# Kernel optimization log

Measured on AMD Instinct MI355X. Metric: run time of the kernel, lower is better.

The kernel has to match this reference:

```python
import jax, jax.numpy as jnp
import numpy as np

# NF4 codebook (bitsandbytes)
NF4 = jnp.array([-1.0, -0.6961928009986877, -0.5250730514526367, -0.39491748809814453,
                 -0.28444138169288635, -0.18477343022823334, -0.09105003625154495, 0.0,
                 0.07958029955625534, 0.16093020141124725, 0.24611230194568634,
                 0.33791524171829224, 0.44070982933044434, 0.5626170039176941,
                 0.7229568362236023, 1.0], dtype=jnp.float32)
BLOCK = 64  # quantization blocksize along the input dim


def _dequant(codes, scales):
    # codes: [O, I] int in [0,16); scales: [O, I//BLOCK] per-block absmax
    w = NF4[codes]                                   # [O, I]
    O, I = w.shape
    w = w.reshape(O, I // BLOCK, BLOCK) * scales[:, :, None]
    return w.reshape(O, I)


def _lin_lora(x, W, A, B):
    # base int4 linear + low-rank adapter: x @ W.T + (x @ A.T) @ B.T
    base = jnp.einsum('bsh,oh->bso', x, W)
    lora = jnp.einsum('bsr,or->bso', jnp.einsum('bsh,rh->bsr', x, A), B)
    return base + lora


def setup_inputs() -> dict:
    H, I, R, BT, S = 4096, 14336, 16, 2, 2048
    key = jax.random.key(0)
    ks = jax.random.split(key, 12)
    x = jax.random.normal(ks[0], (BT, S, H), jnp.float32)
    codes_attn = jax.random.randint(ks[1], (4, H, H), 0, 16, jnp.int32)
    scales_attn = jax.random.uniform(ks[2], (4, H, H // BLOCK), jnp.float32) * 0.02
    codes_gu = jax.random.randint(ks[3], (2, I, H), 0, 16, jnp.int32)
    scales_gu = jax.random.uniform(ks[4], (2, I, H // BLOCK), jnp.float32) * 0.02
    codes_down = jax.random.randint(ks[5], (H, I), 0, 16, jnp.int32)
    scales_down = jax.random.uniform(ks[6], (H, I // BLOCK), jnp.float32) * 0.02
    lora_A_h = jax.random.normal(ks[7], (6, R, H), jnp.float32) * 0.02
    lora_A_down = jax.random.normal(ks[8], (R, I), jnp.float32) * 0.02
    lora_B_attn = jax.random.normal(ks[9], (4, H, R), jnp.float32) * 0.02
    lora_B_gu = jax.random.normal(ks[10], (2, I, R), jnp.float32) * 0.02
    lora_B_down = jax.random.normal(ks[11], (H, R), jnp.float32) * 0.02
    return dict(x=x, codes_attn=codes_attn, scales_attn=scales_attn,
                codes_gu=codes_gu, scales_gu=scales_gu,
                codes_down=codes_down, scales_down=scales_down,
                lora_A_h=lora_A_h, lora_A_down=lora_A_down,
                lora_B_attn=lora_B_attn, lora_B_gu=lora_B_gu,
                lora_B_down=lora_B_down)


def reference(x, codes_attn, scales_attn, codes_gu, scales_gu, codes_down,
              scales_down, lora_A_h, lora_A_down, lora_B_attn, lora_B_gu,
              lora_B_down):
    # attention projections (q, k, v)
    q = _lin_lora(x, _dequant(codes_attn[0], scales_attn[0]), lora_A_h[0], lora_B_attn[0])
    k = _lin_lora(x, _dequant(codes_attn[1], scales_attn[1]), lora_A_h[1], lora_B_attn[1])
    v = _lin_lora(x, _dequant(codes_attn[2], scales_attn[2]), lora_A_h[2], lora_B_attn[2])
    attn = (q + k + v) / 3.0
    o = _lin_lora(attn, _dequant(codes_attn[3], scales_attn[3]), lora_A_h[3], lora_B_attn[3])
    x1 = x + o
    # MLP: silu(gate) * up -> down
    g = _lin_lora(x1, _dequant(codes_gu[0], scales_gu[0]), lora_A_h[4], lora_B_gu[0])
    u = _lin_lora(x1, _dequant(codes_gu[1], scales_gu[1]), lora_A_h[5], lora_B_gu[1])
    h = jax.nn.silu(g) * u
    d = _lin_lora(h, _dequant(codes_down, scales_down), lora_A_down, lora_B_down)
    return x1 + d
```

## Files before the change

kernel.cpp:

```cpp
#include <hip/hip_runtime.h>
#include <cstdint>


typedef __attribute__((ext_vector_type(4))) float f32x4;
typedef __attribute__((ext_vector_type(8))) short s16x8;
typedef __attribute__((ext_vector_type(4))) int   i32x4;

__constant__ float NF4_TBL[16] = {
  -1.0f, -0.6961928009986877f, -0.5250730514526367f, -0.39491748809814453f,
  -0.28444138169288635f, -0.18477343022823334f, -0.09105003625154495f, 0.0f,
   0.07958029955625534f, 0.16093020141124725f, 0.24611230194568634f,
   0.33791524171829224f, 0.44070982933044434f, 0.5626170039176941f,
   0.7229568362236023f, 1.0f };

__device__ __forceinline__ unsigned short f2bf(float f){
  unsigned u = __builtin_bit_cast(unsigned, f);
  u += 0x7fffu + ((u >> 16) & 1u);
  return (unsigned short)(u >> 16);
}
__device__ __forceinline__ float bf2f(unsigned short h){
  return __builtin_bit_cast(float, ((unsigned)h) << 16);
}

__device__ __forceinline__ void gll16(const unsigned short* g, unsigned short* l){
  __builtin_amdgcn_global_load_lds((__attribute__((address_space(1))) unsigned int*)g,
                                   (__attribute__((address_space(3))) unsigned int*)l,
                                   16, 0, 0);
}

__global__ void cast_f32_bf16(unsigned short* __restrict__ dst,
                              const float* __restrict__ src, long long n8){
  const long long i = (long long)blockIdx.x * blockDim.x + threadIdx.x;
  if (i >= n8) return;
  const f32x4 a = *(const f32x4*)(src + i*8);
  const f32x4 b = *(const f32x4*)(src + i*8 + 4);
  s16x8 o;
  o[0]=(short)f2bf(a.x); o[1]=(short)f2bf(a.y); o[2]=(short)f2bf(a.z); o[3]=(short)f2bf(a.w);
  o[4]=(short)f2bf(b.x); o[5]=(short)f2bf(b.y); o[6]=(short)f2bf(b.z); o[7]=(short)f2bf(b.w);
  *(s16x8*)(dst + i*8) = o;
}

__global__ void pack_bl_kernel(unsigned short* __restrict__ dst,
                               const float* __restrict__ src,
                               int N, int coloff, float mul){
  const int i = blockIdx.x * blockDim.x + threadIdx.x;
  if (i >= N * 16) return;
  const int n = i >> 4, r = i & 15;
  dst[(size_t)n * 64 + coloff + r] = f2bf(src[i] * mul);
}

__global__ void dequant1_kernel(unsigned short* __restrict__ dst,
                                const int* __restrict__ codes,
                                const float* __restrict__ scales, int K, float mul){
  const int k = (blockIdx.x * blockDim.x + threadIdx.x) * 8;
  if (k >= K) return;
  const size_t n = blockIdx.y;
  const size_t base = n * (size_t)K + k;
  const float s = scales[n * (size_t)(K >> 6) + (k >> 6)] * mul;
  const i32x4 c0 = *(const i32x4*)(codes + base);
  const i32x4 c1 = *(const i32x4*)(codes + base + 4);
  s16x8 o;
  o[0]=(short)f2bf(NF4_TBL[c0.x]*s); o[1]=(short)f2bf(NF4_TBL[c0.y]*s);
  o[2]=(short)f2bf(NF4_TBL[c0.z]*s); o[3]=(short)f2bf(NF4_TBL[c0.w]*s);
  o[4]=(short)f2bf(NF4_TBL[c1.x]*s); o[5]=(short)f2bf(NF4_TBL[c1.y]*s);
  o[6]=(short)f2bf(NF4_TBL[c1.z]*s); o[7]=(short)f2bf(NF4_TBL[c1.w]*s);
  *(s16x8*)(dst + base) = o;
}

__global__ void dequant3_kernel(unsigned short* __restrict__ dst,
                                const int* __restrict__ codes,
                                const float* __restrict__ scales, int K, float mul){
  const int k = (blockIdx.x * blockDim.x + threadIdx.x) * 8;
  if (k >= K) return;
  const size_t n = blockIdx.y;
  const size_t base = n * (size_t)K + k;
  const size_t CS = (size_t)4096 * 4096;
  const size_t SS = (size_t)4096 * 64;
  float acc[8] = {0.f,0.f,0.f,0.f,0.f,0.f,0.f,0.f};
  #pragma unroll
  for (int t = 0; t < 3; ++t){
    const float s = scales[t * SS + n * (size_t)(K >> 6) + (k >> 6)];
    const i32x4 c0 = *(const i32x4*)(codes + t * CS + base);
    const i32x4 c1 = *(const i32x4*)(codes + t * CS + base + 4);
    acc[0]+=NF4_TBL[c0.x]*s; acc[1]+=NF4_TBL[c0.y]*s; acc[2]+=NF4_TBL[c0.z]*s; acc[3]+=NF4_TBL[c0.w]*s;
    acc[4]+=NF4_TBL[c1.x]*s; acc[5]+=NF4_TBL[c1.y]*s; acc[6]+=NF4_TBL[c1.z]*s; acc[7]+=NF4_TBL[c1.w]*s;
  }
  s16x8 o;
  #pragma unroll
  for (int e = 0; e < 8; ++e) o[e] = (short)f2bf(acc[e] * mul);
  *(s16x8*)(dst + base) = o;
}

template<int NP>
__global__ __launch_bounds__(256)
void lora_t_kernel(const unsigned short* __restrict__ act,
                   const unsigned short* __restrict__ Ab,
                   unsigned short* __restrict__ tout, int K, int coloff){
  __shared__ float red[4][NP][4][64];
  const int tid = threadIdx.x, lane = tid & 63, wave = tid >> 6;
  const int m0 = blockIdx.x * 16;
  const int q = lane >> 4, r = lane & 15;
  const int KW = K >> 2;
  const int kbase = wave * KW;
  const unsigned short* ap = act + (size_t)(m0 + r) * K + kbase + q * 8;
  const unsigned short* bp[NP];
  #pragma unroll
  for (int p = 0; p < NP; ++p)
    bp[p] = Ab + (size_t)(p * 16 + r) * K + kbase + q * 8;
  f32x4 acc[NP];
  #pragma unroll
  for (int p = 0; p < NP; ++p) acc[p] = (f32x4){0.f,0.f,0.f,0.f};
  for (int k = 0; k < KW; k += 32){
    const s16x8 a = *(const s16x8*)ap; ap += 32;
    #pragma unroll
    for (int p = 0; p < NP; ++p){
      const s16x8 b = *(const s16x8*)bp[p]; bp[p] += 32;
      acc[p] = __builtin_amdgcn_mfma_f32_16x16x32_bf16(a, b, acc[p], 0, 0, 0);
    }
  }
  #pragma unroll
  for (int p = 0; p < NP; ++p)
    #pragma unroll
    for (int rr = 0; rr < 4; ++rr) red[wave][p][rr][lane] = acc[p][rr];
  __syncthreads();
  const int rr = tid >> 6, li = tid & 63;
  #pragma unroll
  for (int p = 0; p < NP; ++p){
    const float v = red[0][p][rr][li] + red[1][p][rr][li]
                  + red[2][p][rr][li] + red[3][p][rr][li];
    const int row = m0 + (li >> 4) * 4 + rr;
    const int col = coloff + p * 16 + (li & 15);
    tout[(size_t)row * 64 + col] = f2bf(v);
  }
}

__global__ void silu_mul_kernel(unsigned short* __restrict__ h,
                                const unsigned short* __restrict__ gu){
  const int k8 = blockIdx.x * blockDim.x + threadIdx.x;
  const size_t row = blockIdx.y;
  const s16x8 g8 = *(const s16x8*)(gu + row * 28672 + (size_t)k8 * 8);
  const s16x8 u8 = *(const s16x8*)(gu + row * 28672 + 14336 + (size_t)k8 * 8);
  s16x8 o;
  #pragma unroll
  for (int e = 0; e < 8; ++e){
    const float g = bf2f((unsigned short)g8[e]);
    const float u = bf2f((unsigned short)u8[e]);
    const float s = g / (1.f + __expf(-g));
    o[e] = (short)f2bf(s * u);
  }
  *(s16x8*)(h + row * 14336 + (size_t)k8 * 8) = o;
}

template<int EPI>
__global__ __launch_bounds__(256)
void gemm_kernel(const unsigned short* __restrict__ Aact,
                 const unsigned short* __restrict__ Bw,
                 const unsigned short* __restrict__ tL,
                 const unsigned short* __restrict__ bL,
                 int K, int ldC,
                 const float* __restrict__ resIn,
                 float* __restrict__ outF,
                 unsigned short* __restrict__ outB){
  __shared__ unsigned short As[128 * 64];
  __shared__ unsigned short Bs[128 * 64];
  const int tid  = threadIdx.x;
  const int lane = tid & 63;
  const int wave = tid >> 6;
  const int m0 = blockIdx.x << 7;
  const int n0 = blockIdx.y << 7;

  const int srow  = tid >> 3;
  const int scol  = tid & 7;
  const int swcol = scol ^ (srow & 7);
  const unsigned short* gA = Aact + (size_t)(m0 + srow) * K + swcol * 8;
  const unsigned short* gB = Bw   + (size_t)(n0 + srow) * K + swcol * 8;
  const int ldsbase = wave * 512;

  const int wm = wave >> 1, wn = wave & 1;
  const int q = lane >> 4, r15 = lane & 15;
  int aoff[4][2], boff[4][2];
  #pragma unroll
  for (int i = 0; i < 4; ++i){
    const int ml = wm*64 + i*16 + r15;
    const int nl = wn*64 + i*16 + r15;
    #pragma unroll
    for (int kk = 0; kk < 2; ++kk){
      aoff[i][kk] = ml*64 + ((((kk<<2)|q) ^ (ml & 7)) * 8);
      boff[i][kk] = nl*64 + ((((kk<<2)|q) ^ (nl & 7)) * 8);
    }
  }

  f32x4 acc[4][4];
  #pragma unroll
  for (int i = 0; i < 4; ++i)
    #pragma unroll
    for (int j = 0; j < 4; ++j) acc[i][j] = (f32x4){0.f,0.f,0.f,0.f};

  const int nK = K >> 6;
  size_t koff = 0;
  for (int kt = 0; kt <= nK; ++kt){
    const unsigned short* pa; const unsigned short* pb; size_t rs;
    if (kt < nK){ pa = gA + koff; pb = gB + koff; rs = (size_t)K * 32; }
    else {
      pa = tL + (size_t)(m0 + srow) * 64 + swcol * 8;
      pb = bL + (size_t)(n0 + srow) * 64 + swcol * 8;
      rs = 64 * 32;
    }
    #pragma unroll
    for (int p = 0; p < 4; ++p){
      gll16(pa + rs * p, As + ldsbase + p * 2048);
      gll16(pb + rs * p, Bs + ldsbase + p * 2048);
    }
    __syncthreads();
    #pragma unroll
    for (int kk = 0; kk < 2; ++kk){
      s16x8 af[4], bfr[4];
      #pragma unroll
      for (int i = 0; i < 4; ++i) af[i]  = *(const s16x8*)(As + aoff[i][kk]);
      #pragma unroll
      for (int j = 0; j < 4; ++j) bfr[j] = *(const s16x8*)(Bs + boff[j][kk]);
      #pragma unroll
      for (int i = 0; i < 4; ++i)
        #pragma unroll
        for (int j = 0; j < 4; ++j)
          acc[i][j] = __builtin_amdgcn_mfma_f32_16x16x32_bf16(af[i], bfr[j], acc[i][j], 0, 0, 0);
    }
    __syncthreads();
    koff += 64;
  }

  #pragma unroll
  for (int i = 0; i < 4; ++i){
    const int gm = m0 + wm*64 + i*16 + q*4;
    #pragma unroll
    for (int j = 0; j < 4; ++j){
      const int gn = n0 + wn*64 + j*16 + r15;
      #pragma unroll
      for (int rr = 0; rr < 4; ++rr){
        const size_t idx = (size_t)(gm + rr) * ldC + gn;
        const float v = acc[i][j][rr];
        if constexpr (EPI == 0){
          outB[idx] = f2bf(v);
        } else if constexpr (EPI == 1){
          const float x1 = resIn[idx] + v;
          outF[idx] = x1;
          outB[idx] = f2bf(x1);
        } else {
          outF[idx] = resIn[idx] + v;
        }
      }
    }
  }
}

extern "C" void kernel_launch(void* const* d_in, const int* in_sizes, int n_in,
                              void* d_out, int out_size, void* d_ws, size_t ws_size,
                              hipStream_t stream){
  (void)in_sizes; (void)n_in; (void)out_size; (void)ws_size;
  constexpr int M = 4096, H = 4096, I = 14336, I2 = 28672;

  const float* x            = (const float*)d_in[0];
  const int*   codes_attn   = (const int*)  d_in[1];
  const float* scales_attn  = (const float*)d_in[2];
  const int*   codes_gu     = (const int*)  d_in[3];
  const float* scales_gu    = (const float*)d_in[4];
  const int*   codes_down   = (const int*)  d_in[5];
  const float* scales_down  = (const float*)d_in[6];
  const float* lora_A_h     = (const float*)d_in[7];
  const float* lora_A_down  = (const float*)d_in[8];
  const float* lora_B_attn  = (const float*)d_in[9];
  const float* lora_B_gu    = (const float*)d_in[10];
  const float* lora_B_down  = (const float*)d_in[11];
  float* out = (float*)d_out;

  char* ws = (char*)d_ws;
  size_t off = 0;
  auto take = [&](size_t b){ void* p = ws + off; off += b; return p; };
  unsigned short* xb    = (unsigned short*)take((size_t)M*H*2);
  unsigned short* W1    = (unsigned short*)take((size_t)H*H*2);
  unsigned short* attn  = (unsigned short*)take((size_t)M*H*2);
  float*          x1f   = (float*)         take((size_t)M*H*4);
  unsigned short* x1b   = (unsigned short*)take((size_t)M*H*2);
  unsigned short* Wgu   = (unsigned short*)take((size_t)I2*H*2);
  unsigned short* gu    = (unsigned short*)take((size_t)M*I2*2);
  unsigned short* hbuf  = (unsigned short*)take((size_t)M*I*2);
  unsigned short* t1    = (unsigned short*)take((size_t)M*64*2);
  unsigned short* t2    = (unsigned short*)take((size_t)M*64*2);
  unsigned short* t3    = (unsigned short*)take((size_t)M*64*2);
  unsigned short* t4    = (unsigned short*)take((size_t)M*64*2);
  unsigned short* bl_at = (unsigned short*)take((size_t)H*64*2);
  unsigned short* bl_o  = (unsigned short*)take((size_t)H*64*2);
  unsigned short* bl_gu = (unsigned short*)take((size_t)I2*64*2);
  unsigned short* bl_dn = (unsigned short*)take((size_t)H*64*2);
  const size_t zbytes = (size_t)((char*)ws + off - (char*)t1);
  unsigned short* al_h  = (unsigned short*)take((size_t)6*16*H*2);
  unsigned short* al_dn = (unsigned short*)take((size_t)16*I*2);

  hipMemsetAsync(t1, 0, zbytes, stream);

  cast_f32_bf16<<<dim3((M*(size_t)H/8)/256), 256, 0, stream>>>(xb, x, (long long)M*H/8);
  cast_f32_bf16<<<dim3(192), 256, 0, stream>>>(al_h,  lora_A_h,    (long long)6*16*H/8);
  cast_f32_bf16<<<dim3(112), 256, 0, stream>>>(al_dn, lora_A_down, (long long)16*I/8);

  for (int p = 0; p < 3; ++p)
    pack_bl_kernel<<<dim3(256), 256, 0, stream>>>(bl_at, lora_B_attn + (size_t)p*H*16, H, p*16, 1.f/3.f);
  pack_bl_kernel<<<dim3(256), 256, 0, stream>>>(bl_o, lora_B_attn + (size_t)3*H*16, H, 0, 1.f);
  pack_bl_kernel<<<dim3(896), 256, 0, stream>>>(bl_gu, lora_B_gu, I, 0, 1.f);
  pack_bl_kernel<<<dim3(896), 256, 0, stream>>>(bl_gu + (size_t)I*64, lora_B_gu + (size_t)I*16, I, 16, 1.f);
  pack_bl_kernel<<<dim3(256), 256, 0, stream>>>(bl_dn, lora_B_down, H, 0, 1.f);

  lora_t_kernel<3><<<dim3(M/16), 256, 0, stream>>>(xb, al_h, t1, H, 0);

  dequant3_kernel<<<dim3(H/2048, H), 256, 0, stream>>>(W1, codes_attn, scales_attn, H, 1.f/3.f);
  gemm_kernel<0><<<dim3(32, 32), 256, 0, stream>>>(xb, W1, t1, bl_at, H, H, nullptr, nullptr, attn);

  dequant1_kernel<<<dim3(H/2048, H), 256, 0, stream>>>(W1, codes_attn + (size_t)3*H*H,
                                                       scales_attn + (size_t)3*H*64, H, 1.f);
  lora_t_kernel<1><<<dim3(M/16), 256, 0, stream>>>(attn, al_h + (size_t)3*16*H, t2, H, 0);
  gemm_kernel<1><<<dim3(32, 32), 256, 0, stream>>>(attn, W1, t2, bl_o, H, H, x, x1f, x1b);

  lora_t_kernel<2><<<dim3(M/16), 256, 0, stream>>>(x1b, al_h + (size_t)4*16*H, t3, H, 0);
  dequant1_kernel<<<dim3(H/2048, I2), 256, 0, stream>>>(Wgu, codes_gu, scales_gu, H, 1.f);
  gemm_kernel<0><<<dim3(32, 224), 256, 0, stream>>>(x1b, Wgu, t3, bl_gu, H, I2, nullptr, nullptr, gu);

  silu_mul_kernel<<<dim3(I/2048, M), 256, 0, stream>>>(hbuf, gu);

  lora_t_kernel<1><<<dim3(M/16), 256, 0, stream>>>(hbuf, al_dn, t4, I, 0);
  dequant1_kernel<<<dim3(I/2048, H), 256, 0, stream>>>(Wgu, codes_down, scales_down, I, 1.f);
  gemm_kernel<2><<<dim3(32, 32), 256, 0, stream>>>(hbuf, Wgu, t4, bl_dn, I, H, x1f, out, nullptr);
}
```

Measured before the change: 3.221 ms.

## Fuse SiLU-mul into gate/up GEMM and overlap dequant with GEMMs

Gate and up weight rows are interleaved so the SiLU(g)*u product can be formed in the GEMM epilogue through a lane shuffle. This removes the separate full-size gu buffer and the silu_mul pass. The standalone dequant kernels for Wo, Wgu and Wdown are folded into extra grid rows of the preceding GEMM launches, so weight dequantization runs alongside matrix work. The cost is more workspace, because W1 is enlarged and a separate W2 is added, plus possible imbalance between GEMM tiles and dequant blocks.

```diff
diff --git a/kernel.cpp b/kernel.cpp
--- a/kernel.cpp
+++ b/kernel.cpp
@@ -26,6 +26,36 @@
   __builtin_amdgcn_global_load_lds((__attribute__((address_space(1))) unsigned int*)g,
                                    (__attribute__((address_space(3))) unsigned int*)l,
                                    16, 0, 0);
+}
+
+struct DeqP {
+  unsigned short* dst;
+  const int* c0; const int* c1;
+  const float* s0; const float* s1;
+  int K; int rows; int ilv;
+};
+
+__device__ void deq_rows(const DeqP& p, int bid, int nb){
+  const int K8 = p.K >> 3;
+  for (int n = bid; n < p.rows; n += nb){
+    const int plane = p.ilv ? (n & 1) : 0;
+    const int sr    = p.ilv ? (n >> 1) : n;
+    const int*   cp = (plane ? p.c1 : p.c0) + (size_t)sr * p.K;
+    const float* sp = (plane ? p.s1 : p.s0) + (size_t)sr * (p.K >> 6);
+    unsigned short* dp = p.dst + (size_t)n * p.K;
+    for (int k8 = threadIdx.x; k8 < K8; k8 += 256){
+      const int k = k8 * 8;
+      const float s = sp[k >> 6];
+      const i32x4 c0 = *(const i32x4*)(cp + k);
+      const i32x4 c1 = *(const i32x4*)(cp + k + 4);
+      s16x8 o;
+      o[0]=(short)f2bf(NF4_TBL[c0.x]*s); o[1]=(short)f2bf(NF4_TBL[c0.y]*s);
+      o[2]=(short)f2bf(NF4_TBL[c0.z]*s); o[3]=(short)f2bf(NF4_TBL[c0.w]*s);
+      o[4]=(short)f2bf(NF4_TBL[c1.x]*s); o[5]=(short)f2bf(NF4_TBL[c1.y]*s);
+      o[6]=(short)f2bf(NF4_TBL[c1.z]*s); o[7]=(short)f2bf(NF4_TBL[c1.w]*s);
+      *(s16x8*)(dp + k) = o;
+    }
+  }
 }
 
 __global__ void cast_f32_bf16(unsigned short* __restrict__ dst,
@@ -42,29 +72,11 @@
 
 __global__ void pack_bl_kernel(unsigned short* __restrict__ dst,
                                const float* __restrict__ src,
-                               int N, int coloff, float mul){
+                               int N, int coloff, float mul, int rmul, int radd){
   const int i = blockIdx.x * blockDim.x + threadIdx.x;
   if (i >= N * 16) return;
   const int n = i >> 4, r = i & 15;
-  dst[(size_t)n * 64 + coloff + r] = f2bf(src[i] * mul);
-}
-
-__global__ void dequant1_kernel(unsigned short* __restrict__ dst,
-                                const int* __restrict__ codes,
-                                const float* __restrict__ scales, int K, float mul){
-  const int k = (blockIdx.x * blockDim.x + threadIdx.x) * 8;
-  if (k >= K) return;
-  const size_t n = blockIdx.y;
-  const size_t base = n * (size_t)K + k;
-  const float s = scales[n * (size_t)(K >> 6) + (k >> 6)] * mul;
-  const i32x4 c0 = *(const i32x4*)(codes + base);
-  const i32x4 c1 = *(const i32x4*)(codes + base + 4);
-  s16x8 o;
-  o[0]=(short)f2bf(NF4_TBL[c0.x]*s); o[1]=(short)f2bf(NF4_TBL[c0.y]*s);
-  o[2]=(short)f2bf(NF4_TBL[c0.z]*s); o[3]=(short)f2bf(NF4_TBL[c0.w]*s);
-  o[4]=(short)f2bf(NF4_TBL[c1.x]*s); o[5]=(short)f2bf(NF4_TBL[c1.y]*s);
-  o[6]=(short)f2bf(NF4_TBL[c1.z]*s); o[7]=(short)f2bf(NF4_TBL[c1.w]*s);
-  *(s16x8*)(dst + base) = o;
+  dst[(size_t)(n * rmul + radd) * 64 + coloff + r] = f2bf(src[i] * mul);
 }
 
 __global__ void dequant3_kernel(unsigned short* __restrict__ dst,
@@ -134,23 +146,6 @@
   }
 }
 
-__global__ void silu_mul_kernel(unsigned short* __restrict__ h,
-                                const unsigned short* __restrict__ gu){
-  const int k8 = blockIdx.x * blockDim.x + threadIdx.x;
-  const size_t row = blockIdx.y;
-  const s16x8 g8 = *(const s16x8*)(gu + row * 28672 + (size_t)k8 * 8);
-  const s16x8 u8 = *(const s16x8*)(gu + row * 28672 + 14336 + (size_t)k8 * 8);
-  s16x8 o;
-  #pragma unroll
-  for (int e = 0; e < 8; ++e){
-    const float g = bf2f((unsigned short)g8[e]);
-    const float u = bf2f((unsigned short)u8[e]);
-    const float s = g / (1.f + __expf(-g));
-    o[e] = (short)f2bf(s * u);
-  }
-  *(s16x8*)(h + row * 14336 + (size_t)k8 * 8) = o;
-}
-
 template<int EPI>
 __global__ __launch_bounds__(256)
 void gemm_kernel(const unsigned short* __restrict__ Aact,
@@ -160,7 +155,15 @@
                  int K, int ldC,
                  const float* __restrict__ resIn,
                  float* __restrict__ outF,
-                 unsigned short* __restrict__ outB){
+                 unsigned short* __restrict__ outB,
+                 int NY, DeqP dqa, DeqP dqb){
+  if ((int)blockIdx.y >= NY){
+    const int bid = ((int)blockIdx.y - NY) * gridDim.x + blockIdx.x;
+    const int nb  = ((int)gridDim.y - NY) * gridDim.x;
+    if (dqa.rows) deq_rows(dqa, bid, nb);
+    if (dqb.rows) deq_rows(dqb, bid, nb);
+    return;
+  }
   __shared__ unsigned short As[128 * 64];
   __shared__ unsigned short Bs[128 * 64];
   const int tid  = threadIdx.x;
@@ -237,16 +240,24 @@
       const int gn = n0 + wn*64 + j*16 + r15;
       #pragma unroll
       for (int rr = 0; rr < 4; ++rr){
-        const size_t idx = (size_t)(gm + rr) * ldC + gn;
         const float v = acc[i][j][rr];
-        if constexpr (EPI == 0){
-          outB[idx] = f2bf(v);
-        } else if constexpr (EPI == 1){
-          const float x1 = resIn[idx] + v;
-          outF[idx] = x1;
-          outB[idx] = f2bf(x1);
+        if constexpr (EPI == 3){
+          const float other = __shfl_xor(v, 1);
+          if ((r15 & 1) == 0){
+            const float sg = v / (1.f + __expf(-v));
+            outB[(size_t)(gm + rr) * ldC + (gn >> 1)] = f2bf(sg * other);
+          }
         } else {
-          outF[idx] = resIn[idx] + v;
+          const size_t idx = (size_t)(gm + rr) * ldC + gn;
+          if constexpr (EPI == 0){
+            outB[idx] = f2bf(v);
+          } else if constexpr (EPI == 1){
+            const float x1 = resIn[idx] + v;
+            outF[idx] = x1;
+            outB[idx] = f2bf(x1);
+          } else {
+            outF[idx] = resIn[idx] + v;
+          }
         }
       }
     }
@@ -258,6 +269,7 @@
                               hipStream_t stream){
   (void)in_sizes; (void)n_in; (void)out_size; (void)ws_size;
   constexpr int M = 4096, H = 4096, I = 14336, I2 = 28672;
+  constexpr int IH = 7168;
 
   const float* x            = (const float*)d_in[0];
   const int*   codes_attn   = (const int*)  d_in[1];
@@ -277,12 +289,12 @@
   size_t off = 0;
   auto take = [&](size_t b){ void* p = ws + off; off += b; return p; };
   unsigned short* xb    = (unsigned short*)take((size_t)M*H*2);
-  unsigned short* W1    = (unsigned short*)take((size_t)H*H*2);
+  unsigned short* W1    = (unsigned short*)take((size_t)H*I*2);
+  unsigned short* W2    = (unsigned short*)take((size_t)H*H*2);
   unsigned short* attn  = (unsigned short*)take((size_t)M*H*2);
   float*          x1f   = (float*)         take((size_t)M*H*4);
   unsigned short* x1b   = (unsigned short*)take((size_t)M*H*2);
   unsigned short* Wgu   = (unsigned short*)take((size_t)I2*H*2);
-  unsigned short* gu    = (unsigned short*)take((size_t)M*I2*2);
   unsigned short* hbuf  = (unsigned short*)take((size_t)M*I*2);
   unsigned short* t1    = (unsigned short*)take((size_t)M*64*2);
   unsigned short* t2    = (unsigned short*)take((size_t)M*64*2);
@@ -303,29 +315,42 @@
   cast_f32_bf16<<<dim3(112), 256, 0, stream>>>(al_dn, lora_A_down, (long long)16*I/8);
 
   for (int p = 0; p < 3; ++p)
-    pack_bl_kernel<<<dim3(256), 256, 0, stream>>>(bl_at, lora_B_attn + (size_t)p*H*16, H, p*16, 1.f/3.f);
-  pack_bl_kernel<<<dim3(256), 256, 0, stream>>>(bl_o, lora_B_attn + (size_t)3*H*16, H, 0, 1.f);
-  pack_bl_kernel<<<dim3(896), 256, 0, stream>>>(bl_gu, lora_B_gu, I, 0, 1.f);
-  pack_bl_kernel<<<dim3(896), 256, 0, stream>>>(bl_gu + (size_t)I*64, lora_B_gu + (size_t)I*16, I, 16, 1.f);
-  pack_bl_kernel<<<dim3(256), 256, 0, stream>>>(bl_dn, lora_B_down, H, 0, 1.f);
+    pack_bl_kernel<<<dim3(256), 256, 0, stream>>>(bl_at, lora_B_attn + (size_t)p*H*16, H, p*16, 1.f/3.f, 1, 0);
+  pack_bl_kernel<<<dim3(256), 256, 0, stream>>>(bl_o, lora_B_attn + (size_t)3*H*16, H, 0, 1.f, 1, 0);
+  pack_bl_kernel<<<dim3(896), 256, 0, stream>>>(bl_gu, lora_B_gu, I, 0, 1.f, 2, 0);
+  pack_bl_kernel<<<dim3(896), 256, 0, stream>>>(bl_gu, lora_B_gu + (size_t)I*16, I, 16, 1.f, 2, 1);
+  pack_bl_kernel<<<dim3(256), 256, 0, stream>>>(bl_dn, lora_B_down, H, 0, 1.f, 1, 0);
+
+  dequant3_kernel<<<dim3(H/2048, H), 256, 0, stream>>>(W1, codes_attn, scales_attn, H, 1.f/3.f);
 
   lora_t_kernel<3><<<dim3(M/16), 256, 0, stream>>>(xb, al_h, t1, H, 0);
 
-  dequant3_kernel<<<dim3(H/2048, H), 256, 0, stream>>>(W1, codes_attn, scales_attn, H, 1.f/3.f);
-  gemm_kernel<0><<<dim3(32, 32), 256, 0, stream>>>(xb, W1, t1, bl_at, H, H, nullptr, nullptr, attn);
-
-  dequant1_kernel<<<dim3(H/2048, H), 256, 0, stream>>>(W1, codes_attn + (size_t)3*H*H,
-                                                       scales_attn + (size_t)3*H*64, H, 1.f);
+  const DeqP dq0{};
+  {
+    DeqP dWo { W2, codes_attn + (size_t)3*H*H, nullptr,
+               scales_attn + (size_t)3*H*64, nullptr, H, H, 0 };
+    DeqP dGuA{ Wgu, codes_gu, codes_gu + (size_t)I*H,
+               scales_gu, scales_gu + (size_t)I*64, H, I, 1 };
+    gemm_kernel<0><<<dim3(32, 64), 256, 0, stream>>>(xb, W1, t1, bl_at, H, H,
+                                                     nullptr, nullptr, attn, 32, dWo, dGuA);
+  }
+
   lora_t_kernel<1><<<dim3(M/16), 256, 0, stream>>>(attn, al_h + (size_t)3*16*H, t2, H, 0);
-  gemm_kernel<1><<<dim3(32, 32), 256, 0, stream>>>(attn, W1, t2, bl_o, H, H, x, x1f, x1b);
+  {
+    DeqP dGuB{ Wgu + (size_t)I*H, codes_gu + (size_t)IH*H, codes_gu + (size_t)I*H + (size_t)IH*H,
+               scales_gu + (size_t)IH*64, scales_gu + (size_t)I*64 + (size_t)IH*64, H, I, 1 };
+    gemm_kernel<1><<<dim3(32, 64), 256, 0, stream>>>(attn, W2, t2, bl_o, H, H,
+                                                     x, x1f, x1b, 32, dGuB, dq0);
+  }
 
   lora_t_kernel<2><<<dim3(M/16), 256, 0, stream>>>(x1b, al_h + (size_t)4*16*H, t3, H, 0);
-  dequant1_kernel<<<dim3(H/2048, I2), 256, 0, stream>>>(Wgu, codes_gu, scales_gu, H, 1.f);
-  gemm_kernel<0><<<dim3(32, 224), 256, 0, stream>>>(x1b, Wgu, t3, bl_gu, H, I2, nullptr, nullptr, gu);
-
-  silu_mul_kernel<<<dim3(I/2048, M), 256, 0, stream>>>(hbuf, gu);
+  {
+    DeqP dWd { W1, codes_down, nullptr, scales_down, nullptr, I, H, 0 };
+    gemm_kernel<3><<<dim3(32, 224 + 32), 256, 0, stream>>>(x1b, Wgu, t3, bl_gu, H, I,
+                                                           nullptr, nullptr, hbuf, 224, dWd, dq0);
+  }
 
   lora_t_kernel<1><<<dim3(M/16), 256, 0, stream>>>(hbuf, al_dn, t4, I, 0);
-  dequant1_kernel<<<dim3(I/2048, H), 256, 0, stream>>>(Wgu, codes_down, scales_down, I, 1.f);
-  gemm_kernel<2><<<dim3(32, 32), 256, 0, stream>>>(hbuf, Wgu, t4, bl_dn, I, H, x1f, out, nullptr);
-}
+  gemm_kernel<2><<<dim3(32, 32), 256, 0, stream>>>(hbuf, W1, t4, bl_dn, I, H,
+                                                   x1f, out, nullptr, 32, dq0, dq0);
+}
```

Measured after the change: 3.172 ms. No clear change (-1.5%).
